# Performance work log

Hardware: AMD Instinct MI355X
Metric: run time of the kernel (lower is better)

The kernel has to match this reference:

```python
import jax, jax.numpy as jnp
import numpy as np

EPS = 1e-6
C = 1.0
ITERS = 10
P = 128   # number of prototype groups
B = 4096
D = 128


def expmap0(v, c=C):
    n = jnp.maximum(jnp.linalg.norm(v, axis=-1, keepdims=True), EPS)
    sc = c ** 0.5
    return v * (jnp.tanh(sc * n) / (sc * n))


def mobius_add(x, y, c=C):
    x2 = jnp.sum(x * x, axis=-1, keepdims=True)
    y2 = jnp.sum(y * y, axis=-1, keepdims=True)
    xy = jnp.sum(x * y, axis=-1, keepdims=True)
    cxy2 = 2.0 * c * xy
    num = (1.0 + cxy2 + c * y2) * x + (1.0 - c * x2) * y
    den = 1.0 + cxy2 + c * c * x2 * y2
    return num / jnp.maximum(den, EPS)


def project_to_ball(x, c=C, eps=1e-5):
    # factor computed under no_grad in the original -> stop_gradient
    norm = jnp.maximum(jnp.linalg.norm(x, axis=-1, keepdims=True), EPS)
    max_norm = (1.0 - eps) / c ** 0.5
    factor = jnp.minimum(jnp.ones_like(norm), max_norm / norm)
    return x * jax.lax.stop_gradient(factor)


def group_poincare_mean(x, masks, c=C, iters=ITERS):
    # x: [B, D] points on the ball; masks: [P, B] float group membership
    cnt = jnp.maximum(jnp.sum(masks, axis=-1, keepdims=True), 1.0)  # [P, 1]
    mu = (masks @ x) / cnt                                           # [P, D] Euclidean init
    mu = project_to_ball(mu, c)
    for _ in range(iters):
        diff = mobius_add(x[None, :, :], -mu[:, None, :], c)        # [P, B, D]
        mdiff = jnp.einsum('pb,pbd->pd', masks, diff) / cnt          # masked mean per group
        mu = project_to_ball(mobius_add(mu, mdiff, c), c)
    return mu


def poincare_distance_matrix(x, c=C):
    # x: [P, D]
    x2 = jnp.sum(x * x, axis=-1, keepdims=True)                      # [P, 1]
    diff = x[:, None, :] - x[None, :, :]                             # [P, P, D]
    dist2 = jnp.sum(diff * diff, axis=-1)                            # [P, P]
    sc = c ** 0.5
    num = 2.0 * sc * dist2
    a = jnp.maximum(1.0 - c * x2, EPS)                               # [P, 1]
    denom = a @ a.T                                                  # [P, P]
    z = 1.0 + num / jnp.maximum(denom, EPS)
    return jnp.arccosh(jnp.maximum(z, 1.0 + EPS))


def setup_inputs() -> dict:
    key = jax.random.key(0)
    k1, k2, k3 = jax.random.split(key, 3)
    representations = jax.random.normal(k1, (B, D), dtype=jnp.float32)
    targets = jax.random.randint(k2, (B,), 0, P, dtype=jnp.int64)
    n_pairs = P * (P - 1) // 2
    dT = jax.random.randint(k3, (n_pairs,), 0, 12, dtype=jnp.int32)
    return {"representations": representations, "targets": targets, "dT": dT}


def reference(representations, targets, dT):
    # group membership masks [P, B]
    masks = (targets[None, :] == jnp.arange(P, dtype=targets.dtype)[:, None]).astype(representations.dtype)
    reps_p = expmap0(representations, C)                 # map to Poincare ball
    prototypes = group_poincare_mean(reps_p, masks, C)   # [P, D]
    prototypes = project_to_ball(prototypes, C)
    dB_matrix = poincare_distance_matrix(prototypes, C)  # [P, P]
    iu, ju = np.triu_indices(P, k=1)
    dB = dB_matrix[iu, ju]                               # [P*(P-1)/2]
    dT_f = dT.astype(dB.dtype)
    # Pearson correlation (torch.corrcoef)
    a = dB - jnp.mean(dB)
    b = dT_f - jnp.mean(dT_f)
    corr = jnp.sum(a * b) / jnp.sqrt(jnp.sum(a * a) * jnp.sum(b * b))
    return jnp.where(jnp.isnan(corr), jnp.asarray(1.0, dB.dtype), 1.0 - corr)
```

## Files before the change

kernel.cpp:

```cpp
#include <hip/hip_runtime.h>
#include <math.h>

#define EPSF    1e-6f
#define B_N     4096
#define P_N     128
#define D_N     128
#define NPAIRS  (P_N * (P_N - 1) / 2)
#define ITERS   10
#define MAXNORM 0.99999f
#define MCAP    512
#define WCAP    128
#define SLOTS   64

template <int CTRL>
__device__ __forceinline__ float dppadd(float x) {
    float t = __int_as_float(__builtin_amdgcn_update_dpp(
        0, __float_as_int(x), CTRL, 0xf, 0xf, true));
    return x + t;
}
__device__ __forceinline__ float red8(float x) {
    x = dppadd<0xB1>(x);
    x = dppadd<0x4E>(x);
    x = dppadd<0x141>(x);
    return x;
}
__device__ __forceinline__ float wsum64(float x) {
    x = dppadd<0x111>(x); x = dppadd<0x112>(x); x = dppadd<0x114>(x);
    x = dppadd<0x118>(x); x = dppadd<0x142>(x); x = dppadd<0x143>(x);
    return __int_as_float(__builtin_amdgcn_readlane(__float_as_int(x), 63));
}
__device__ __forceinline__ void wsum64_2(float& a, float& b) {
#define DPP_STEP(ctrl) \
    a = dppadd<ctrl>(a); b = dppadd<ctrl>(b);
    DPP_STEP(0x111) DPP_STEP(0x112) DPP_STEP(0x114) DPP_STEP(0x118) DPP_STEP(0x142) DPP_STEP(0x143)
#undef DPP_STEP
    a = __int_as_float(__builtin_amdgcn_readlane(__float_as_int(a), 63));
    b = __int_as_float(__builtin_amdgcn_readlane(__float_as_int(b), 63));
}
__device__ __forceinline__ double wred64d(double v) {
    v += __shfl_xor(v, 1);  v += __shfl_xor(v, 2);  v += __shfl_xor(v, 4);
    v += __shfl_xor(v, 8);  v += __shfl_xor(v, 16); v += __shfl_xor(v, 32);
    return v;
}
__device__ __forceinline__ float rlane(float v, int l) {
    return __int_as_float(__builtin_amdgcn_readlane(__float_as_int(v), l));
}
__device__ __forceinline__ float dot16(const float4* r, const float4* m) {
    float d = 0.f;
#pragma unroll
    for (int j = 0; j < 4; ++j)
        d += r[j].x * m[j].x + r[j].y * m[j].y + r[j].z * m[j].z + r[j].w * m[j].w;
    return d;
}
__device__ __forceinline__ float tanh_fast(float x) {
    float t = __expf(-2.0f * x);
    return (1.0f - t) / (1.0f + t);
}

__global__ __launch_bounds__(256) void proto_kernel(
        const float* __restrict__ reps,
        const int*   __restrict__ targets,
        float* __restrict__ mu_out,
        float* __restrict__ mu2_out,
        int*   __restrict__ counter) {
    __shared__ int    wtmp[4][WCAP];
    __shared__ int    wcnt[4];
    __shared__ int    woff[4];
    __shared__ int    mlist[MCAP];
    __shared__ int    s_n;
    __shared__ float4 xs4[SLOTS * 32];
    __shared__ float  sc_l[MCAP];
    __shared__ float  x2_l[MCAP];
    __shared__ float  w_l[MCAP];
    __shared__ float  cb_l[MCAP];
    __shared__ float  mu_lds[D_N];
    __shared__ float  part[2][4][D_N];
    __shared__ float  scbp[2][4];

    const int p    = blockIdx.x;
    const int tid  = threadIdx.x;
    const int wv   = tid >> 6;
    const int lane = tid & 63;
    const int grp  = lane >> 3;
    const int q    = lane & 7;

    if (p == 0 && tid == 0) counter[0] = 0;

    {
        int tg[16];
#pragma unroll
        for (int r = 0; r < 16; ++r) tg[r] = targets[(wv << 10) + (r << 6) + lane];
        const unsigned long long lowmask = (1ULL << lane) - 1ULL;
        int cnt = 0;
#pragma unroll
        for (int r = 0; r < 16; ++r) {
            bool mm = (tg[r] == p);
            unsigned long long mk = __ballot(mm);
            if (mm) {
                int pos = cnt + __popcll(mk & lowmask);
                if (pos < WCAP) wtmp[wv][pos] = (wv << 10) + (r << 6) + lane;
            }
            cnt += __popcll(mk);
        }
        if (cnt > WCAP) cnt = WCAP;
        if (lane == 0) wcnt[wv] = cnt;
    }
    __syncthreads();
    if (tid == 0) {
        int c0 = wcnt[0], c1 = wcnt[1], c2 = wcnt[2], c3 = wcnt[3];
        woff[0] = 0; woff[1] = c0; woff[2] = c0 + c1; woff[3] = c0 + c1 + c2;
        int nn = c0 + c1 + c2 + c3;
        s_n = (nn > MCAP) ? MCAP : nn;
    }
    __syncthreads();
    {
        int base = woff[wv], cnt = wcnt[wv];
        for (int i = lane; i < cnt; i += 64) mlist[base + i] = wtmp[wv][i];
    }
    __syncthreads();

    const int   n       = s_n;
    const float inv_cnt = 1.0f / fmaxf((float)n, 1.0f);
    const float4* reps4 = (const float4*)reps;
    const float2* reps2 = (const float2*)reps;

    const int mA = wv * 16 + grp;
    const int mB = mA + 8;

    float4 rA[4], rB[4];
    float  x2A, x2B;
    {
        bool act = (mA < n);
        int  b   = act ? mlist[mA] : 0;
        float ss = 0.f;
#pragma unroll
        for (int j = 0; j < 4; ++j) {
            rA[j] = reps4[(size_t)b * 32 + 4 * q + j];
            ss += rA[j].x * rA[j].x + rA[j].y * rA[j].y + rA[j].z * rA[j].z + rA[j].w * rA[j].w;
        }
        ss = red8(ss);
        float nn = fmaxf(sqrtf(ss), EPSF);
        float sv = act ? (tanh_fast(nn) / nn) : 0.f;
#pragma unroll
        for (int j = 0; j < 4; ++j) {
            rA[j].x *= sv; rA[j].y *= sv; rA[j].z *= sv; rA[j].w *= sv;
            xs4[mA * 32 + ((4 * q + j) ^ (mA & 7))] = rA[j];
        }
        x2A = act ? ss * sv * sv : 0.f;
    }
    {
        bool act = (mB < n);
        int  b   = act ? mlist[mB] : 0;
        float ss = 0.f;
#pragma unroll
        for (int j = 0; j < 4; ++j) {
            rB[j] = reps4[(size_t)b * 32 + 4 * q + j];
            ss += rB[j].x * rB[j].x + rB[j].y * rB[j].y + rB[j].z * rB[j].z + rB[j].w * rB[j].w;
        }
        ss = red8(ss);
        float nn = fmaxf(sqrtf(ss), EPSF);
        float sv = act ? (tanh_fast(nn) / nn) : 0.f;
#pragma unroll
        for (int j = 0; j < 4; ++j) {
            rB[j].x *= sv; rB[j].y *= sv; rB[j].z *= sv; rB[j].w *= sv;
            xs4[mB * 32 + ((4 * q + j) ^ (mB & 7))] = rB[j];
        }
        x2B = act ? ss * sv * sv : 0.f;
    }
    for (int mb = SLOTS + wv * 16; mb < n; mb += 64) {
#pragma unroll
        for (int t = 0; t < 2; ++t) {
            int  m   = mb + grp + 8 * t;
            bool act = (m < n);
            int  b   = act ? mlist[m] : 0;
            float ss = 0.f;
#pragma unroll
            for (int j = 0; j < 4; ++j) {
                float4 t4 = reps4[(size_t)b * 32 + 4 * q + j];
                ss += t4.x * t4.x + t4.y * t4.y + t4.z * t4.z + t4.w * t4.w;
            }
            ss = red8(ss);
            if (act && q == 0) {
                float nn = fmaxf(sqrtf(ss), EPSF);
                float sv = tanh_fast(nn) / nn;
                sc_l[m] = sv;
                x2_l[m] = ss * sv * sv;
            }
        }
    }

    const float* xsf = (const float*)xs4;
    const int    lh  = lane >> 1, lb = (lane & 1) * 2;
    float2 xd[16];
#pragma unroll
    for (int k = 0; k < 16; ++k) {
        int m = wv * 16 + k;
        xd[k] = *(const float2*)&xsf[(m * 32 + (lh ^ (m & 7))) * 4 + lb];
    }

    {
        float2 S; S.x = 0.f; S.y = 0.f;
#pragma unroll
        for (int k = 0; k < 16; ++k) { S.x += xd[k].x; S.y += xd[k].y; }
        for (int mb = SLOTS + wv * 16; mb < n; mb += 64) {
            for (int k = 0; k < 16; ++k) {
                int m = mb + k;
                if (m < n) {
                    float2 rv = reps2[(size_t)mlist[m] * 64 + lane];
                    float s = sc_l[m];
                    S.x += s * rv.x; S.y += s * rv.y;
                }
            }
        }
        *(float2*)&part[1][wv][2 * lane] = S;
    }
    __syncthreads();
    float2 muf; float mu2;
    {
        float2 T; T.x = 0.f; T.y = 0.f;
#pragma unroll
        for (int w2 = 0; w2 < 4; ++w2) {
            float2 pv = *(const float2*)&part[1][w2][2 * lane];
            T.x += pv.x; T.y += pv.y;
        }
        muf.x = T.x * inv_cnt; muf.y = T.y * inv_cnt;
        float m2  = wsum64(muf.x * muf.x + muf.y * muf.y);
        float nrm = fmaxf(sqrtf(m2), EPSF);
        float fac = fminf(1.0f, MAXNORM / nrm);
        muf.x *= fac; muf.y *= fac;
        mu2 = m2 * fac * fac;
        *(float2*)&mu_lds[2 * lane] = muf;
    }

    for (int it = 0; it < ITERS; ++it) {
        const int buf = it & 1;
        const float4* mu4 = (const float4*)mu_lds;
        float4 ms[4];
#pragma unroll
        for (int j = 0; j < 4; ++j) ms[j] = mu4[4 * q + j];

        float wA, cbA, wB, cbB;
        {
            float d   = red8(dot16(rA, ms));
            float ca  = 1.0f - 2.0f * d + mu2;
            float cbv = 1.0f - x2A;
            float den = fmaxf(1.0f - 2.0f * d + x2A * mu2, EPSF);
            float iv  = 1.0f / den;
            bool  act = (mA < n);
            wA  = act ? ca * iv : 0.f;
            cbA = act ? cbv * iv : 0.f;
        }
        {
            float d   = red8(dot16(rB, ms));
            float ca  = 1.0f - 2.0f * d + mu2;
            float cbv = 1.0f - x2B;
            float den = fmaxf(1.0f - 2.0f * d + x2B * mu2, EPSF);
            float iv  = 1.0f / den;
            bool  act = (mB < n);
            wB  = act ? ca * iv : 0.f;
            cbB = act ? cbv * iv : 0.f;
        }
        for (int mb = SLOTS + wv * 16; mb < n; mb += 64) {
#pragma unroll
            for (int t = 0; t < 2; ++t) {
                int  m   = mb + grp + 8 * t;
                bool act = (m < n);
                int  b   = act ? mlist[m] : 0;
                float dd = 0.f;
#pragma unroll
                for (int j = 0; j < 4; ++j) {
                    float4 a = reps4[(size_t)b * 32 + 4 * q + j];
                    dd += a.x * ms[j].x + a.y * ms[j].y + a.z * ms[j].z + a.w * ms[j].w;
                }
                dd = red8(dd);
                if (act) {
                    float dp  = sc_l[m] * dd;
                    float x2v = x2_l[m];
                    float ca  = 1.0f - 2.0f * dp + mu2;
                    float cbv = 1.0f - x2v;
                    float den = fmaxf(1.0f - 2.0f * dp + x2v * mu2, EPSF);
                    float iv  = 1.0f / den;
                    if (q == 0) { w_l[m] = ca * iv; cb_l[m] = cbv * iv; }
                }
            }
        }

        float2 S2; S2.x = 0.f; S2.y = 0.f;
        float  scb = 0.f;
#pragma unroll
        for (int k = 0; k < 8; ++k) {
            float wk = rlane(wA, 8 * k);
            float ck = rlane(cbA, 8 * k);
            S2.x += wk * xd[k].x; S2.y += wk * xd[k].y;
            scb  += ck;
        }
#pragma unroll
        for (int k = 0; k < 8; ++k) {
            float wk = rlane(wB, 8 * k);
            float ck = rlane(cbB, 8 * k);
            S2.x += wk * xd[8 + k].x; S2.y += wk * xd[8 + k].y;
            scb  += ck;
        }
        for (int mb = SLOTS + wv * 16; mb < n; mb += 64) {
            for (int k = 0; k < 16; ++k) {
                int m = mb + k;
                if (m < n) {
                    float wvv = w_l[m] * sc_l[m];
                    scb += cb_l[m];
                    float2 rv = reps2[(size_t)mlist[m] * 64 + lane];
                    S2.x += wvv * rv.x; S2.y += wvv * rv.y;
                }
            }
        }
        *(float2*)&part[buf][wv][2 * lane] = S2;
        if (lane == 0) scbp[buf][wv] = scb;
        __syncthreads();

        float2 T; T.x = 0.f; T.y = 0.f;
#pragma unroll
        for (int w2 = 0; w2 < 4; ++w2) {
            float2 pv = *(const float2*)&part[buf][w2][2 * lane];
            T.x += pv.x; T.y += pv.y;
        }
        float scbt = scbp[buf][0] + scbp[buf][1] + scbp[buf][2] + scbp[buf][3];
        float scs  = scbt * inv_cnt;
        float2 md;
        md.x = T.x * inv_cnt - scs * muf.x;
        md.y = T.y * inv_cnt - scs * muf.y;

        float A0 = md.x * md.x + md.y * md.y;
        float A1 = muf.x * md.x + muf.y * md.y;
        wsum64_2(A0, A1);
        float ca  = 1.0f + 2.0f * A1 + A0;
        float cbv = 1.0f - mu2;
        float den = fmaxf(1.0f + 2.0f * A1 + mu2 * A0, EPSF);
        float iv  = 1.0f / den;
        float2 tv;
        tv.x = (ca * muf.x + cbv * md.x) * iv;
        tv.y = (ca * muf.y + cbv * md.y) * iv;
        float t2   = (ca * ca * mu2 + 2.0f * ca * cbv * A1 + cbv * cbv * A0) * iv * iv;
        float nrm2 = fmaxf(sqrtf(t2), EPSF);
        float fc   = fminf(1.0f, MAXNORM / nrm2);
        muf.x = tv.x * fc; muf.y = tv.y * fc;
        mu2   = t2 * fc * fc;
        *(float2*)&mu_lds[2 * lane] = muf;
    }

    {
        float nf = fmaxf(sqrtf(mu2), EPSF);
        float ff = fminf(1.0f, MAXNORM / nf);
        muf.x *= ff; muf.y *= ff;
        mu2 = mu2 * ff * ff;
    }
    if (wv == 0) {
        ((float2*)(mu_out + (size_t)p * D_N))[lane] = muf;
        if (lane == 0) mu2_out[p] = mu2;
    }
}

__global__ __launch_bounds__(1024) void distcorr_kernel(
        const float* __restrict__ mu,
        const float* __restrict__ mu2s,
        const int*   __restrict__ dT,
        double* __restrict__ gpart,
        int*    __restrict__ counter,
        float*  __restrict__ out) {
    __shared__ float  lmu[P_N * 129];
    __shared__ float  lmu2[P_N];
    __shared__ double sh[16][5];
    __shared__ int    s_last;

    const int tid = threadIdx.x;
#pragma unroll
    for (int e = 0; e < 16; ++e) {
        int idx = tid + e * 1024;
        lmu[(idx >> 7) * 129 + (idx & 127)] = mu[idx];
    }
    if (tid < P_N) lmu2[tid] = mu2s[tid];
    __syncthreads();

    int k = blockIdx.x * 1024 + tid;
    double p0 = 0.0, p1 = 0.0, p2 = 0.0, p3 = 0.0, p4 = 0.0;
    if (k < NPAIRS) {
        int i = (int)(127.5f - sqrtf(127.5f * 127.5f - 2.0f * (float)k));
        if (i < 0) i = 0;
        while ((i + 1) * (2 * P_N - i - 2) / 2 <= k) ++i;
        while (i * (2 * P_N - i - 1) / 2 > k) --i;
        int j = k - i * (2 * P_N - i - 1) / 2 + i + 1;

        const float* ra = &lmu[i * 129];
        const float* rb = &lmu[j * 129];
        float a0 = 0.f, a1 = 0.f, a2 = 0.f, a3 = 0.f;
#pragma unroll
        for (int d = 0; d < D_N; d += 4) {
            float f0 = ra[d]     - rb[d];
            float f1 = ra[d + 1] - rb[d + 1];
            float f2 = ra[d + 2] - rb[d + 2];
            float f3 = ra[d + 3] - rb[d + 3];
            a0 += f0 * f0; a1 += f1 * f1; a2 += f2 * f2; a3 += f3 * f3;
        }
        float d2 = (a0 + a1) + (a2 + a3);
        float ai = fmaxf(1.f - lmu2[i], EPSF);
        float aj = fmaxf(1.f - lmu2[j], EPSF);
        float z  = 1.f + 2.f * d2 / fmaxf(ai * aj, EPSF);
        z = fmaxf(z, 1.f + EPSF);
        float dist = __logf(z + sqrtf(z * z - 1.f));
        double bb = (double)dist;
        double tt = (double)dT[k];
        p0 = bb; p1 = bb * bb; p2 = tt; p3 = tt * tt; p4 = bb * tt;
    }
    p0 = wred64d(p0); p1 = wred64d(p1); p2 = wred64d(p2);
    p3 = wred64d(p3); p4 = wred64d(p4);
    const int wid = tid >> 6, lane = tid & 63;
    if (lane == 0) {
        sh[wid][0] = p0; sh[wid][1] = p1; sh[wid][2] = p2;
        sh[wid][3] = p3; sh[wid][4] = p4;
    }
    __syncthreads();
    if (tid == 0) {
        double b0 = 0, b1 = 0, b2 = 0, b3 = 0, b4 = 0;
        for (int w = 0; w < 16; ++w) {
            b0 += sh[w][0]; b1 += sh[w][1]; b2 += sh[w][2];
            b3 += sh[w][3]; b4 += sh[w][4];
        }
        double* gp = gpart + (size_t)blockIdx.x * 5;
        gp[0] = b0; gp[1] = b1; gp[2] = b2; gp[3] = b3; gp[4] = b4;
        __threadfence();
        int old = atomicAdd(counter, 1);
        s_last = (old == (int)gridDim.x - 1) ? 1 : 0;
    }
    __syncthreads();
    if (!s_last) return;
    if (tid == 0) {
        __threadfence();
        double t0 = 0, t1 = 0, t2 = 0, t3 = 0, t4 = 0;
        for (int b = 0; b < 8; ++b) {
            t0 += gpart[b * 5 + 0]; t1 += gpart[b * 5 + 1]; t2 += gpart[b * 5 + 2];
            t3 += gpart[b * 5 + 3]; t4 += gpart[b * 5 + 4];
        }
        const double nn = (double)NPAIRS;
        double mb  = t0 / nn;
        double mt  = t2 / nn;
        double cov = t4 - nn * mb * mt;
        double vb  = t1 - nn * mb * mb;
        double vt  = t3 - nn * mt * mt;
        double corr = cov / sqrt(vb * vt);
        double res  = isnan(corr) ? 1.0 : (1.0 - corr);
        out[0] = (float)res;
    }
}

extern "C" void kernel_launch(void* const* d_in, const int* in_sizes, int n_in,
                              void* d_out, int out_size, void* d_ws, size_t ws_size,
                              hipStream_t stream) {
    const float* reps    = (const float*)d_in[0];
    const int*   targets = (const int*)d_in[1];
    const int*   dT      = (const int*)d_in[2];
    float* out = (float*)d_out;

    double* gpart   = (double*)d_ws;
    int*    counter = (int*)((char*)d_ws + 320);
    float*  mu      = (float*)((char*)d_ws + 384);
    float*  mu2s    = mu + (size_t)P_N * D_N;

    proto_kernel<<<P_N, 256, 0, stream>>>(reps, targets, mu, mu2s, counter);
    distcorr_kernel<<<8, 1024, 0, stream>>>(mu, mu2s, dT, gpart, counter, out);
}
```

Measured before the change: 28.04 us.

## Spread distance-correlation over more blocks and read prototypes directly from global

```diff
diff --git a/kernel.cpp b/kernel.cpp
--- a/kernel.cpp
+++ b/kernel.cpp
@@ -11,6 +11,8 @@
 #define MCAP    512
 #define WCAP    128
 #define SLOTS   64
+#define DBLK    32
+#define PPB     254
 
 template <int CTRL>
 __device__ __forceinline__ float dppadd(float x) {
@@ -358,50 +360,41 @@
     }
 }
 
-__global__ __launch_bounds__(1024) void distcorr_kernel(
+__global__ __launch_bounds__(256) void distcorr_kernel(
         const float* __restrict__ mu,
         const float* __restrict__ mu2s,
         const int*   __restrict__ dT,
         double* __restrict__ gpart,
         int*    __restrict__ counter,
         float*  __restrict__ out) {
-    __shared__ float  lmu[P_N * 129];
-    __shared__ float  lmu2[P_N];
-    __shared__ double sh[16][5];
+    __shared__ double sh[4][5];
     __shared__ int    s_last;
 
-    const int tid = threadIdx.x;
-#pragma unroll
-    for (int e = 0; e < 16; ++e) {
-        int idx = tid + e * 1024;
-        lmu[(idx >> 7) * 129 + (idx & 127)] = mu[idx];
-    }
-    if (tid < P_N) lmu2[tid] = mu2s[tid];
-    __syncthreads();
-
-    int k = blockIdx.x * 1024 + tid;
+    const int tid  = threadIdx.x;
+    const int wid  = tid >> 6;
+    const int lane = tid & 63;
+    const int k    = blockIdx.x * PPB + tid;
+
     double p0 = 0.0, p1 = 0.0, p2 = 0.0, p3 = 0.0, p4 = 0.0;
-    if (k < NPAIRS) {
+    if (tid < PPB) {
         int i = (int)(127.5f - sqrtf(127.5f * 127.5f - 2.0f * (float)k));
         if (i < 0) i = 0;
         while ((i + 1) * (2 * P_N - i - 2) / 2 <= k) ++i;
         while (i * (2 * P_N - i - 1) / 2 > k) --i;
         int j = k - i * (2 * P_N - i - 1) / 2 + i + 1;
 
-        const float* ra = &lmu[i * 129];
-        const float* rb = &lmu[j * 129];
+        const float4* ra = (const float4*)(mu + (size_t)i * D_N);
+        const float4* rb = (const float4*)(mu + (size_t)j * D_N);
         float a0 = 0.f, a1 = 0.f, a2 = 0.f, a3 = 0.f;
 #pragma unroll
-        for (int d = 0; d < D_N; d += 4) {
-            float f0 = ra[d]     - rb[d];
-            float f1 = ra[d + 1] - rb[d + 1];
-            float f2 = ra[d + 2] - rb[d + 2];
-            float f3 = ra[d + 3] - rb[d + 3];
+        for (int d = 0; d < 32; ++d) {
+            float4 a = ra[d], b = rb[d];
+            float f0 = a.x - b.x, f1 = a.y - b.y, f2 = a.z - b.z, f3 = a.w - b.w;
             a0 += f0 * f0; a1 += f1 * f1; a2 += f2 * f2; a3 += f3 * f3;
         }
         float d2 = (a0 + a1) + (a2 + a3);
-        float ai = fmaxf(1.f - lmu2[i], EPSF);
-        float aj = fmaxf(1.f - lmu2[j], EPSF);
+        float ai = fmaxf(1.f - mu2s[i], EPSF);
+        float aj = fmaxf(1.f - mu2s[j], EPSF);
         float z  = 1.f + 2.f * d2 / fmaxf(ai * aj, EPSF);
         z = fmaxf(z, 1.f + EPSF);
         float dist = __logf(z + sqrtf(z * z - 1.f));
@@ -411,7 +404,6 @@
     }
     p0 = wred64d(p0); p1 = wred64d(p1); p2 = wred64d(p2);
     p3 = wred64d(p3); p4 = wred64d(p4);
-    const int wid = tid >> 6, lane = tid & 63;
     if (lane == 0) {
         sh[wid][0] = p0; sh[wid][1] = p1; sh[wid][2] = p2;
         sh[wid][3] = p3; sh[wid][4] = p4;
@@ -419,7 +411,8 @@
     __syncthreads();
     if (tid == 0) {
         double b0 = 0, b1 = 0, b2 = 0, b3 = 0, b4 = 0;
-        for (int w = 0; w < 16; ++w) {
+#pragma unroll
+        for (int w = 0; w < 4; ++w) {
             b0 += sh[w][0]; b1 += sh[w][1]; b2 += sh[w][2];
             b3 += sh[w][3]; b4 += sh[w][4];
         }
@@ -431,22 +424,27 @@
     }
     __syncthreads();
     if (!s_last) return;
-    if (tid == 0) {
-        __threadfence();
-        double t0 = 0, t1 = 0, t2 = 0, t3 = 0, t4 = 0;
-        for (int b = 0; b < 8; ++b) {
-            t0 += gpart[b * 5 + 0]; t1 += gpart[b * 5 + 1]; t2 += gpart[b * 5 + 2];
-            t3 += gpart[b * 5 + 3]; t4 += gpart[b * 5 + 4];
-        }
-        const double nn = (double)NPAIRS;
-        double mb  = t0 / nn;
-        double mt  = t2 / nn;
-        double cov = t4 - nn * mb * mt;
-        double vb  = t1 - nn * mb * mb;
-        double vt  = t3 - nn * mt * mt;
-        double corr = cov / sqrt(vb * vt);
-        double res  = isnan(corr) ? 1.0 : (1.0 - corr);
-        out[0] = (float)res;
+    __threadfence();
+
+    if (tid < 64) {
+        double q0 = 0, q1 = 0, q2 = 0, q3 = 0, q4 = 0;
+        if (lane < DBLK) {
+            const double* gp = gpart + (size_t)lane * 5;
+            q0 = gp[0]; q1 = gp[1]; q2 = gp[2]; q3 = gp[3]; q4 = gp[4];
+        }
+        q0 = wred64d(q0); q1 = wred64d(q1); q2 = wred64d(q2);
+        q3 = wred64d(q3); q4 = wred64d(q4);
+        if (tid == 0) {
+            const double nn = (double)NPAIRS;
+            double mb  = q0 / nn;
+            double mt  = q2 / nn;
+            double cov = q4 - nn * mb * mt;
+            double vb  = q1 - nn * mb * mb;
+            double vt  = q3 - nn * mt * mt;
+            double corr = cov / sqrt(vb * vt);
+            double res  = isnan(corr) ? 1.0 : (1.0 - corr);
+            out[0] = (float)res;
+        }
     }
 }
 
@@ -459,10 +457,10 @@
     float* out = (float*)d_out;
 
     double* gpart   = (double*)d_ws;
-    int*    counter = (int*)((char*)d_ws + 320);
-    float*  mu      = (float*)((char*)d_ws + 384);
+    int*    counter = (int*)((char*)d_ws + 1280);
+    float*  mu      = (float*)((char*)d_ws + 1536);
     float*  mu2s    = mu + (size_t)P_N * D_N;
 
     proto_kernel<<<P_N, 256, 0, stream>>>(reps, targets, mu, mu2s, counter);
-    distcorr_kernel<<<8, 1024, 0, stream>>>(mu, mu2s, dT, gpart, counter, out);
-}
+    distcorr_kernel<<<DBLK, 256, 0, stream>>>(mu, mu2s, dT, gpart, counter, out);
+}
```

After: 26.09 us. 7.0% less time.
